# Performance work log

Hardware: AMD Instinct MI355X
Metric: run time of the kernel (lower is better)

## Reference

```python
import jax, jax.numpy as jnp
import numpy as np

D_MODEL = 1024
N_HEAD = 16
D_K = D_MODEL // N_HEAD
FFN = 4096
EPS = 1e-5


def setup_inputs() -> dict:
    key = jax.random.key(0)
    ks = jax.random.split(key, 12)
    s = 0.02
    return {
        "x": jax.random.normal(ks[0], (16, 512, D_MODEL), dtype=jnp.float32),
        "ln1_g": jnp.ones((D_MODEL,), jnp.float32),
        "ln1_b": jnp.zeros((D_MODEL,), jnp.float32),
        "w_q": jax.random.normal(ks[1], (D_MODEL, D_MODEL), jnp.float32) * s,
        "w_k": jax.random.normal(ks[2], (D_MODEL, D_MODEL), jnp.float32) * s,
        "w_v": jax.random.normal(ks[3], (D_MODEL, D_MODEL), jnp.float32) * s,
        "w_o": jax.random.normal(ks[4], (D_MODEL, D_MODEL), jnp.float32) * s,
        "b_o": jnp.zeros((D_MODEL,), jnp.float32),
        "ln2_g": jnp.ones((D_MODEL,), jnp.float32),
        "ln2_b": jnp.zeros((D_MODEL,), jnp.float32),
        "w1": jax.random.normal(ks[5], (D_MODEL, FFN), jnp.float32) * s,
        "b1": jnp.zeros((FFN,), jnp.float32),
        "w2": jax.random.normal(ks[6], (FFN, D_MODEL), jnp.float32) * s,
        "b2": jnp.zeros((D_MODEL,), jnp.float32),
    }


def layernorm(x, g, b):
    mu = jnp.mean(x, axis=-1, keepdims=True)
    var = jnp.mean((x - mu) ** 2, axis=-1, keepdims=True)
    return (x - mu) * jax.lax.rsqrt(var + EPS) * g + b


def reference(x, ln1_g, ln1_b, w_q, w_k, w_v, w_o, b_o, ln2_g, ln2_b, w1, b1, w2, b2):
    B, T, C = x.shape
    # --- attention sublayer (pre-LN) ---
    h = layernorm(x, ln1_g, ln1_b)
    # torch Linear: y = x @ W.T; here weights stored as (in, out) so y = x @ W
    q = (h @ w_q).reshape(B, T, N_HEAD, D_K).transpose(0, 2, 1, 3)  # bhtd
    k = (h @ w_k).reshape(B, T, N_HEAD, D_K).transpose(0, 2, 1, 3)
    v = (h @ w_v).reshape(B, T, N_HEAD, D_K).transpose(0, 2, 1, 3)
    scale = 1.0 / jnp.sqrt(jnp.float32(D_K))
    attn = jnp.einsum("bhqd,bhkd->bhqk", q, k) * scale  # [B,H,T,T]
    causal = jnp.tril(jnp.ones((T, T), bool))
    attn = jnp.where(causal[None, None], attn, -jnp.inf)
    attn = jax.nn.softmax(attn, axis=-1)
    out = jnp.einsum("bhqk,bhkd->bhqd", attn, v)
    out = out.transpose(0, 2, 1, 3).reshape(B, T, C)
    attn_out = out @ w_o + b_o
    x = x + attn_out
    # --- FFN sublayer (pre-LN) ---
    h = layernorm(x, ln2_g, ln2_b)
    ffn_out = jax.nn.gelu(h @ w1 + b1, approximate=False) @ w2 + b2
    return x + ffn_out
```

## Files before the change

### kernel.cpp

```cpp
#include <hip/hip_runtime.h>
#include <hip/hip_bf16.h>
#include <math.h>

#define D_MODEL 1024
#define FFN_DIM 4096
#define NHEAD 16
#define DK 64
#define BATCH 16
#define SEQ 512
#define ROWS (BATCH * SEQ)
#define QKV_N 3072

typedef short short8 __attribute__((ext_vector_type(8)));
typedef float f32x4 __attribute__((ext_vector_type(4)));

__device__ __forceinline__ float bf2f(short s) {
    return __uint_as_float(((unsigned)(unsigned short)s) << 16);
}
__device__ __forceinline__ short f2bf(float f) {
    unsigned u = __float_as_uint(f);
    u += 0x7fff + ((u >> 16) & 1);
    return (short)(u >> 16);
}

__device__ __forceinline__ int swz(int row, int col) {
    int s = (row ^ (row >> 3)) & 7;
    return row * 64 + ((((col >> 3) ^ s) << 3) | (col & 7));
}

__device__ __forceinline__ void gll16(const short* g, short* l) {
    __builtin_amdgcn_global_load_lds(
        (const __attribute__((address_space(1))) unsigned int*)g,
        (__attribute__((address_space(3))) unsigned int*)l, 16, 0, 0);
}

__global__ __launch_bounds__(256) void convT(const float* __restrict__ in,
                                             short* __restrict__ out,
                                             int K, int N) {
    __shared__ short t[64 * 64];
    const int tid = threadIdx.x;
    const int k0 = blockIdx.y * 64, n0 = blockIdx.x * 64;
    {
        const int r = tid >> 4;
        const int c4 = (tid & 15) * 4;
#pragma unroll
        for (int i = 0; i < 4; ++i) {
            const int row = i * 16 + r;
            float4 vv = *(const float4*)&in[(size_t)(k0 + row) * N + n0 + c4];
            t[swz(row, c4 + 0)] = f2bf(vv.x);
            t[swz(row, c4 + 1)] = f2bf(vv.y);
            t[swz(row, c4 + 2)] = f2bf(vv.z);
            t[swz(row, c4 + 3)] = f2bf(vv.w);
        }
    }
    __syncthreads();
    {
        const int n = tid >> 2;
        const int kc = (tid & 3) * 16;
        short tmp[16];
#pragma unroll
        for (int kk = 0; kk < 16; ++kk) tmp[kk] = t[swz(kc + kk, n)];
        short8 s0, s1;
#pragma unroll
        for (int j = 0; j < 8; ++j) { s0[j] = tmp[j]; s1[j] = tmp[8 + j]; }
        short* dst = &out[(size_t)(n0 + n) * K + k0 + kc];
        *(short8*)dst = s0;
        *(short8*)(dst + 8) = s1;
    }
}

__global__ __launch_bounds__(256) void ln_kernel(const float* __restrict__ x,
                                                 const float* __restrict__ g,
                                                 const float* __restrict__ beta,
                                                 short* __restrict__ out) {
    const int row = blockIdx.x;
    const int tid = threadIdx.x;
    const float4 xv = ((const float4*)(x + (size_t)row * D_MODEL))[tid];
    float s  = xv.x + xv.y + xv.z + xv.w;
    float s2 = xv.x * xv.x + xv.y * xv.y + xv.z * xv.z + xv.w * xv.w;
#pragma unroll
    for (int off = 32; off >= 1; off >>= 1) {
        s  += __shfl_down(s, off);
        s2 += __shfl_down(s2, off);
    }
    __shared__ float red[8];
    if ((tid & 63) == 0) { red[(tid >> 6) * 2] = s; red[(tid >> 6) * 2 + 1] = s2; }
    __syncthreads();
    s  = red[0] + red[2] + red[4] + red[6];
    s2 = red[1] + red[3] + red[5] + red[7];
    const float mu  = s * (1.0f / D_MODEL);
    const float var = s2 * (1.0f / D_MODEL) - mu * mu;
    const float r   = rsqrtf(var + 1e-5f);
    const int c = tid * 4;
    short4 ov;
    ov.x = f2bf((xv.x - mu) * r * g[c + 0] + beta[c + 0]);
    ov.y = f2bf((xv.y - mu) * r * g[c + 1] + beta[c + 1]);
    ov.z = f2bf((xv.z - mu) * r * g[c + 2] + beta[c + 2]);
    ov.w = f2bf((xv.w - mu) * r * g[c + 3] + beta[c + 3]);
    *(short4*)(out + (size_t)row * D_MODEL + c) = ov;
}

template <int MODE>
__global__ __launch_bounds__(256) void gemm128(
    const short* __restrict__ A, const short* __restrict__ Bt,
    int M, int N, int K, int ldc,
    const float* __restrict__ bias, const float* __restrict__ resid,
    float* __restrict__ outf, short* __restrict__ outb) {
    __shared__ __align__(16) short As[2][128 * 64];
    __shared__ __align__(16) short Bs[2][128 * 64];
    const int tid = threadIdx.x;
    const int w = tid >> 6, lane = tid & 63;
    const int lm = lane & 15, quad = lane >> 4;
    const int m0 = blockIdx.y * 128, n0 = blockIdx.x * 128;
    const int wm = (w & 1) * 64, wn = (w >> 1) * 64;

    const int srl = lane >> 3;
    const int gch = (lane & 7) ^ srl;
    const short* gA[4];
    const short* gB[4];
    int lofs[4];
#pragma unroll
    for (int j = 0; j < 4; ++j) {
        const int row = j * 32 + w * 8 + srl;
        gA[j] = A  + (size_t)(m0 + row) * K + gch * 8;
        gB[j] = Bt + (size_t)(n0 + row) * K + gch * 8;
        lofs[j] = (j * 32 + w * 8) * 64;
    }

    f32x4 acc[4][4];
#pragma unroll
    for (int i = 0; i < 4; ++i)
#pragma unroll
        for (int j = 0; j < 4; ++j) acc[i][j] = (f32x4){0.f, 0.f, 0.f, 0.f};

#pragma unroll
    for (int j = 0; j < 4; ++j) gll16(gA[j], &As[0][lofs[j]]);
#pragma unroll
    for (int j = 0; j < 4; ++j) gll16(gB[j], &Bs[0][lofs[j]]);

    int buf = 0;
    for (int k0 = 0; k0 < K; k0 += 64) {
        __syncthreads();
        if (k0 + 64 < K) {
#pragma unroll
            for (int j = 0; j < 4; ++j) gll16(gA[j] + k0 + 64, &As[buf ^ 1][lofs[j]]);
#pragma unroll
            for (int j = 0; j < 4; ++j) gll16(gB[j] + k0 + 64, &Bs[buf ^ 1][lofs[j]]);
        }
#pragma unroll
        for (int kk = 0; kk < 2; ++kk) {
            short8 af[4], bfr[4];
#pragma unroll
            for (int mm = 0; mm < 4; ++mm) {
                const int row = wm + mm * 16 + lm;
                const int ch = (kk * 4 + quad) ^ (row & 7);
                af[mm] = *(short8*)&As[buf][row * 64 + ch * 8];
            }
#pragma unroll
            for (int nn = 0; nn < 4; ++nn) {
                const int row = wn + nn * 16 + lm;
                const int ch = (kk * 4 + quad) ^ (row & 7);
                bfr[nn] = *(short8*)&Bs[buf][row * 64 + ch * 8];
            }
#pragma unroll
            for (int mm = 0; mm < 4; ++mm)
#pragma unroll
                for (int nn = 0; nn < 4; ++nn)
                    acc[mm][nn] = __builtin_amdgcn_mfma_f32_16x16x32_bf16(
                        af[mm], bfr[nn], acc[mm][nn], 0, 0, 0);
        }
        buf ^= 1;
    }

#pragma unroll
    for (int mm = 0; mm < 4; ++mm)
#pragma unroll
        for (int nn = 0; nn < 4; ++nn)
#pragma unroll
            for (int r = 0; r < 4; ++r) {
                const int row = m0 + wm + mm * 16 + quad * 4 + r;
                const int col = n0 + wn + nn * 16 + lm;
                const float vv = acc[mm][nn][r];
                if (MODE == 0) {
                    outb[(size_t)row * ldc + col] = f2bf(vv);
                } else if (MODE == 1) {
                    outf[(size_t)row * ldc + col] =
                        vv + bias[col] + resid[(size_t)row * ldc + col];
                } else {
                    const float gv = vv + bias[col];
                    const float u = 0.7978845608f * gv * (1.0f + 0.044715f * gv * gv);
                    const float ge = gv / (1.0f + __expf(-2.0f * u));
                    outb[(size_t)row * ldc + col] = f2bf(ge);
                }
            }
}

__global__ __launch_bounds__(256) void attn_mfma(const short* __restrict__ qkv,
                                                 short* __restrict__ o) {
    __shared__ __align__(16) short Ks[64 * 64];
    __shared__ __align__(16) short Vt[64 * 64];
    __shared__ __align__(16) short Ps[4][32 * 64];

    const int tid = threadIdx.x;
    const int qt = blockIdx.x, h = blockIdx.y, b = blockIdx.z;
    const int w = tid >> 6, lane = tid & 63;
    const int lm = lane & 15, quad = lane >> 4;

    const int sj  = tid >> 2;
    const int sd0 = (tid & 3) * 16;

    short8 aq[2][2];
#pragma unroll
    for (int m = 0; m < 2; ++m) {
        const short* qrow =
            qkv + (size_t)(b * SEQ + qt * 128 + w * 32 + m * 16 + lm) * QKV_N + h * DK;
#pragma unroll
        for (int kk = 0; kk < 2; ++kk) {
            short8 raw = *(const short8*)(qrow + kk * 32 + quad * 8);
            short8 sc;
#pragma unroll
            for (int j = 0; j < 8; ++j) sc[j] = f2bf(bf2f(raw[j]) * 0.125f);
            aq[m][kk] = sc;
        }
    }

    f32x4 accO[2][4];
#pragma unroll
    for (int m = 0; m < 2; ++m)
#pragma unroll
        for (int i = 0; i < 4; ++i) accO[m][i] = (f32x4){0.f, 0.f, 0.f, 0.f};
    float mrow[2][4], lrow[2][4];
#pragma unroll
    for (int m = 0; m < 2; ++m)
#pragma unroll
        for (int r = 0; r < 4; ++r) { mrow[m][r] = -1e30f; lrow[m][r] = 0.f; }

    short* pw = Ps[w];
    const int ktmax = 2 * qt + 1;

    for (int kt = 0; kt <= ktmax; ++kt) {
        __syncthreads();
        {
            const short* ksrc =
                qkv + (size_t)(b * SEQ + kt * 64 + sj) * QKV_N + D_MODEL + h * DK + sd0;
            short8 k0v = *(const short8*)ksrc;
            short8 k1v = *(const short8*)(ksrc + 8);
            *(short8*)&Ks[swz(sj, sd0)]     = k0v;
            *(short8*)&Ks[swz(sj, sd0 + 8)] = k1v;
            const short* vsrc =
                qkv + (size_t)(b * SEQ + kt * 64 + sj) * QKV_N + 2 * D_MODEL + h * DK + sd0;
            short8 v0v = *(const short8*)vsrc;
            short8 v1v = *(const short8*)(vsrc + 8);
#pragma unroll
            for (int dd = 0; dd < 8; ++dd) Vt[swz(sd0 + dd, sj)]     = v0v[dd];
#pragma unroll
            for (int dd = 0; dd < 8; ++dd) Vt[swz(sd0 + 8 + dd, sj)] = v1v[dd];
        }
        __syncthreads();

        bool live[2];
#pragma unroll
        for (int m = 0; m < 2; ++m) {
            const int rowmin = qt * 128 + w * 32 + m * 16;
            live[m] = (kt * 64 <= rowmin + 15);
            if (!live[m]) continue;
            const bool needmask = (kt * 64 + 63 > rowmin);

            f32x4 sacc[4];
#pragma unroll
            for (int nn = 0; nn < 4; ++nn) sacc[nn] = (f32x4){0.f, 0.f, 0.f, 0.f};
#pragma unroll
            for (int kk = 0; kk < 2; ++kk)
#pragma unroll
                for (int nn = 0; nn < 4; ++nn) {
                    short8 bfrag = *(short8*)&Ks[swz(nn * 16 + lm, kk * 32 + quad * 8)];
                    sacc[nn] = __builtin_amdgcn_mfma_f32_16x16x32_bf16(
                        aq[m][kk], bfrag, sacc[nn], 0, 0, 0);
                }

            if (needmask) {
#pragma unroll
                for (int nn = 0; nn < 4; ++nn) {
                    const int kg = kt * 64 + nn * 16 + lm;
#pragma unroll
                    for (int r = 0; r < 4; ++r) {
                        const int qg = rowmin + quad * 4 + r;
                        if (kg > qg) sacc[nn][r] = -1e30f;
                    }
                }
            }

            float mnew[4], alpha[4], rsum[4];
#pragma unroll
            for (int r = 0; r < 4; ++r) {
                float mx = fmaxf(fmaxf(sacc[0][r], sacc[1][r]),
                                 fmaxf(sacc[2][r], sacc[3][r]));
#pragma unroll
                for (int msk = 1; msk <= 8; msk <<= 1) mx = fmaxf(mx, __shfl_xor(mx, msk));
                mnew[r] = fmaxf(mrow[m][r], mx);
                alpha[r] = __expf(mrow[m][r] - mnew[r]);
                rsum[r] = 0.f;
            }
#pragma unroll
            for (int nn = 0; nn < 4; ++nn)
#pragma unroll
                for (int r = 0; r < 4; ++r) {
                    const float p = __expf(sacc[nn][r] - mnew[r]);
                    sacc[nn][r] = p;
                    rsum[r] += p;
                }
#pragma unroll
            for (int r = 0; r < 4; ++r) {
#pragma unroll
                for (int msk = 1; msk <= 8; msk <<= 1) rsum[r] += __shfl_xor(rsum[r], msk);
                lrow[m][r] = lrow[m][r] * alpha[r] + rsum[r];
                mrow[m][r] = mnew[r];
            }
#pragma unroll
            for (int nn = 0; nn < 4; ++nn)
#pragma unroll
                for (int r = 0; r < 4; ++r) accO[m][nn][r] *= alpha[r];

#pragma unroll
            for (int nn = 0; nn < 4; ++nn)
#pragma unroll
                for (int r = 0; r < 4; ++r)
                    pw[swz(m * 16 + quad * 4 + r, nn * 16 + lm)] = f2bf(sacc[nn][r]);
        }

#pragma unroll
        for (int kk = 0; kk < 2; ++kk) {
            short8 bfr[4];
#pragma unroll
            for (int nn = 0; nn < 4; ++nn)
                bfr[nn] = *(short8*)&Vt[swz(nn * 16 + lm, kk * 32 + quad * 8)];
#pragma unroll
            for (int m = 0; m < 2; ++m) {
                if (!live[m]) continue;
                short8 afrag = *(short8*)&pw[swz(m * 16 + lm, kk * 32 + quad * 8)];
#pragma unroll
                for (int nn = 0; nn < 4; ++nn)
                    accO[m][nn] = __builtin_amdgcn_mfma_f32_16x16x32_bf16(
                        afrag, bfr[nn], accO[m][nn], 0, 0, 0);
            }
        }
    }

#pragma unroll
    for (int m = 0; m < 2; ++m)
#pragma unroll
        for (int r = 0; r < 4; ++r) {
            const float invl = 1.0f / lrow[m][r];
            const int row = b * SEQ + qt * 128 + w * 32 + m * 16 + quad * 4 + r;
#pragma unroll
            for (int nn = 0; nn < 4; ++nn)
                o[(size_t)row * D_MODEL + h * DK + nn * 16 + lm] =
                    f2bf(accO[m][nn][r] * invl);
        }
}

extern "C" void kernel_launch(void* const* d_in, const int* in_sizes, int n_in,
                              void* d_out, int out_size, void* d_ws, size_t ws_size,
                              hipStream_t stream) {
    const float* x     = (const float*)d_in[0];
    const float* ln1_g = (const float*)d_in[1];
    const float* ln1_b = (const float*)d_in[2];
    const float* w_q   = (const float*)d_in[3];
    const float* w_k   = (const float*)d_in[4];
    const float* w_v   = (const float*)d_in[5];
    const float* w_o   = (const float*)d_in[6];
    const float* b_o   = (const float*)d_in[7];
    const float* ln2_g = (const float*)d_in[8];
    const float* ln2_b = (const float*)d_in[9];
    const float* w1    = (const float*)d_in[10];
    const float* b1    = (const float*)d_in[11];
    const float* w2    = (const float*)d_in[12];
    const float* b2    = (const float*)d_in[13];
    float* out = (float*)d_out;

    char* ws = (char*)d_ws;
    size_t off = 0;
    auto alloc = [&](size_t bytes) {
        char* p = ws + off;
        off += (bytes + 255) & ~(size_t)255;
        return p;
    };
    short* h_bf   = (short*)alloc((size_t)ROWS * D_MODEL * 2);
    short* qkv_bf = (short*)alloc((size_t)ROWS * QKV_N * 2);
    short* a_bf   = (short*)alloc((size_t)ROWS * D_MODEL * 2);
    float* x1     = (float*)alloc((size_t)ROWS * D_MODEL * 4);
    short* wqkvT  = (short*)alloc((size_t)QKV_N * D_MODEL * 2);
    short* woT    = (short*)alloc((size_t)D_MODEL * D_MODEL * 2);
    short* w1T    = (short*)alloc((size_t)D_MODEL * FFN_DIM * 2);
    short* w2T    = (short*)alloc((size_t)FFN_DIM * D_MODEL * 2);
    short* g1_bf  = qkv_bf;

    convT<<<dim3(16, 16), 256, 0, stream>>>(w_q, wqkvT, D_MODEL, D_MODEL);
    convT<<<dim3(16, 16), 256, 0, stream>>>(w_k, wqkvT + (size_t)D_MODEL * D_MODEL,
                                            D_MODEL, D_MODEL);
    convT<<<dim3(16, 16), 256, 0, stream>>>(w_v, wqkvT + (size_t)2 * D_MODEL * D_MODEL,
                                            D_MODEL, D_MODEL);
    convT<<<dim3(16, 16), 256, 0, stream>>>(w_o, woT, D_MODEL, D_MODEL);
    convT<<<dim3(64, 16), 256, 0, stream>>>(w1, w1T, D_MODEL, FFN_DIM);
    convT<<<dim3(16, 64), 256, 0, stream>>>(w2, w2T, FFN_DIM, D_MODEL);

    ln_kernel<<<ROWS, 256, 0, stream>>>(x, ln1_g, ln1_b, h_bf);

    gemm128<0><<<dim3(QKV_N / 128, ROWS / 128), 256, 0, stream>>>(
        h_bf, wqkvT, ROWS, QKV_N, D_MODEL, QKV_N,
        nullptr, nullptr, nullptr, qkv_bf);

    attn_mfma<<<dim3(SEQ / 128, NHEAD, BATCH), 256, 0, stream>>>(qkv_bf, a_bf);

    gemm128<1><<<dim3(D_MODEL / 128, ROWS / 128), 256, 0, stream>>>(
        a_bf, woT, ROWS, D_MODEL, D_MODEL, D_MODEL, b_o, x, x1, nullptr);

    ln_kernel<<<ROWS, 256, 0, stream>>>(x1, ln2_g, ln2_b, h_bf);

    gemm128<2><<<dim3(FFN_DIM / 128, ROWS / 128), 256, 0, stream>>>(
        h_bf, w1T, ROWS, FFN_DIM, D_MODEL, FFN_DIM, b1, nullptr, nullptr, g1_bf);

    gemm128<1><<<dim3(D_MODEL / 128, ROWS / 128), 256, 0, stream>>>(
        g1_bf, w2T, ROWS, D_MODEL, FFN_DIM, D_MODEL, b2, x1, out, nullptr);
}
```

Before: 511.6 us.

## Pre-shuffle weights into MFMA fragment order and load B directly from global

Weight conversion now writes bf16 weights in a packed per-16-column, per-32-k fragment layout that matches the MFMA B-operand register layout. The GEMM drops the B shared-memory tiles and their async copies and has each lane read its B fragments straight from global memory, one 16-byte load per fragment. This halves LDS usage and removes B staging, which could raise occupancy. The cost is that B reads are no longer shared through LDS between the two waves that use the same columns, and the global loads are issued synchronously inside the inner loop, so their latency is not prefetched a stage ahead.

Result: no change. 504.5 us (-1.4%).

```diff
diff --git a/kernel.cpp b/kernel.cpp
--- a/kernel.cpp
+++ b/kernel.cpp
@@ -34,39 +34,20 @@
         (__attribute__((address_space(3))) unsigned int*)l, 16, 0, 0);
 }
 
-__global__ __launch_bounds__(256) void convT(const float* __restrict__ in,
-                                             short* __restrict__ out,
-                                             int K, int N) {
-    __shared__ short t[64 * 64];
+__global__ __launch_bounds__(256) void convShuf(const float* __restrict__ in,
+                                                short* __restrict__ out,
+                                                int K, int N) {
     const int tid = threadIdx.x;
-    const int k0 = blockIdx.y * 64, n0 = blockIdx.x * 64;
-    {
-        const int r = tid >> 4;
-        const int c4 = (tid & 15) * 4;
-#pragma unroll
-        for (int i = 0; i < 4; ++i) {
-            const int row = i * 16 + r;
-            float4 vv = *(const float4*)&in[(size_t)(k0 + row) * N + n0 + c4];
-            t[swz(row, c4 + 0)] = f2bf(vv.x);
-            t[swz(row, c4 + 1)] = f2bf(vv.y);
-            t[swz(row, c4 + 2)] = f2bf(vv.z);
-            t[swz(row, c4 + 3)] = f2bf(vv.w);
-        }
-    }
-    __syncthreads();
-    {
-        const int n = tid >> 2;
-        const int kc = (tid & 3) * 16;
-        short tmp[16];
-#pragma unroll
-        for (int kk = 0; kk < 16; ++kk) tmp[kk] = t[swz(kc + kk, n)];
-        short8 s0, s1;
-#pragma unroll
-        for (int j = 0; j < 8; ++j) { s0[j] = tmp[j]; s1[j] = tmp[8 + j]; }
-        short* dst = &out[(size_t)(n0 + n) * K + k0 + kc];
-        *(short8*)dst = s0;
-        *(short8*)(dst + 8) = s1;
-    }
+    const int lane = tid & 63, fl = tid >> 6;
+    const int lm = lane & 15, quad = lane >> 4;
+    const int nt = blockIdx.x;
+    const int kc = blockIdx.y * 4 + fl;
+    const int n = nt * 16 + lm;
+    const int kb = kc * 32 + quad * 8;
+    short8 v;
+#pragma unroll
+    for (int j = 0; j < 8; ++j) v[j] = f2bf(in[(size_t)(kb + j) * N + n]);
+    *(short8*)&out[((size_t)nt * (K / 32) + kc) * 512 + lane * 8] = v;
 }
 
 __global__ __launch_bounds__(256) void ln_kernel(const float* __restrict__ x,
@@ -102,31 +83,34 @@
 
 template <int MODE>
 __global__ __launch_bounds__(256) void gemm128(
-    const short* __restrict__ A, const short* __restrict__ Bt,
+    const short* __restrict__ A, const short* __restrict__ Bp,
     int M, int N, int K, int ldc,
     const float* __restrict__ bias, const float* __restrict__ resid,
     float* __restrict__ outf, short* __restrict__ outb) {
     __shared__ __align__(16) short As[2][128 * 64];
-    __shared__ __align__(16) short Bs[2][128 * 64];
     const int tid = threadIdx.x;
     const int w = tid >> 6, lane = tid & 63;
     const int lm = lane & 15, quad = lane >> 4;
     const int m0 = blockIdx.y * 128, n0 = blockIdx.x * 128;
     const int wm = (w & 1) * 64, wn = (w >> 1) * 64;
+    const int KC = K / 32;
 
     const int srl = lane >> 3;
     const int gch = (lane & 7) ^ srl;
     const short* gA[4];
-    const short* gB[4];
     int lofs[4];
 #pragma unroll
     for (int j = 0; j < 4; ++j) {
         const int row = j * 32 + w * 8 + srl;
-        gA[j] = A  + (size_t)(m0 + row) * K + gch * 8;
-        gB[j] = Bt + (size_t)(n0 + row) * K + gch * 8;
+        gA[j] = A + (size_t)(m0 + row) * K + gch * 8;
         lofs[j] = (j * 32 + w * 8) * 64;
     }
 
+    const short* bptr[4];
+#pragma unroll
+    for (int nn = 0; nn < 4; ++nn)
+        bptr[nn] = Bp + ((size_t)((n0 + wn) / 16 + nn) * KC) * 512 + lane * 8;
+
     f32x4 acc[4][4];
 #pragma unroll
     for (int i = 0; i < 4; ++i)
@@ -135,8 +119,6 @@
 
 #pragma unroll
     for (int j = 0; j < 4; ++j) gll16(gA[j], &As[0][lofs[j]]);
-#pragma unroll
-    for (int j = 0; j < 4; ++j) gll16(gB[j], &Bs[0][lofs[j]]);
 
     int buf = 0;
     for (int k0 = 0; k0 < K; k0 += 64) {
@@ -144,23 +126,19 @@
         if (k0 + 64 < K) {
 #pragma unroll
             for (int j = 0; j < 4; ++j) gll16(gA[j] + k0 + 64, &As[buf ^ 1][lofs[j]]);
-#pragma unroll
-            for (int j = 0; j < 4; ++j) gll16(gB[j] + k0 + 64, &Bs[buf ^ 1][lofs[j]]);
         }
 #pragma unroll
         for (int kk = 0; kk < 2; ++kk) {
+            const int kc = (k0 >> 5) + kk;
             short8 af[4], bfr[4];
+#pragma unroll
+            for (int nn = 0; nn < 4; ++nn)
+                bfr[nn] = *(const short8*)(bptr[nn] + (size_t)kc * 512);
 #pragma unroll
             for (int mm = 0; mm < 4; ++mm) {
                 const int row = wm + mm * 16 + lm;
                 const int ch = (kk * 4 + quad) ^ (row & 7);
                 af[mm] = *(short8*)&As[buf][row * 64 + ch * 8];
-            }
-#pragma unroll
-            for (int nn = 0; nn < 4; ++nn) {
-                const int row = wn + nn * 16 + lm;
-                const int ch = (kk * 4 + quad) ^ (row & 7);
-                bfr[nn] = *(short8*)&Bs[buf][row * 64 + ch * 8];
             }
 #pragma unroll
             for (int mm = 0; mm < 4; ++mm)
@@ -389,37 +367,42 @@
     short* qkv_bf = (short*)alloc((size_t)ROWS * QKV_N * 2);
     short* a_bf   = (short*)alloc((size_t)ROWS * D_MODEL * 2);
     float* x1     = (float*)alloc((size_t)ROWS * D_MODEL * 4);
-    short* wqkvT  = (short*)alloc((size_t)QKV_N * D_MODEL * 2);
-    short* woT    = (short*)alloc((size_t)D_MODEL * D_MODEL * 2);
-    short* w1T    = (short*)alloc((size_t)D_MODEL * FFN_DIM * 2);
-    short* w2T    = (short*)alloc((size_t)FFN_DIM * D_MODEL * 2);
+    short* wqkvP  = (short*)alloc((size_t)QKV_N * D_MODEL * 2);
+    short* woP    = (short*)alloc((size_t)D_MODEL * D_MODEL * 2);
+    short* w1P    = (short*)alloc((size_t)D_MODEL * FFN_DIM * 2);
+    short* w2P    = (short*)alloc((size_t)FFN_DIM * D_MODEL * 2);
     short* g1_bf  = qkv_bf;
 
-    convT<<<dim3(16, 16), 256, 0, stream>>>(w_q, wqkvT, D_MODEL, D_MODEL);
-    convT<<<dim3(16, 16), 256, 0, stream>>>(w_k, wqkvT + (size_t)D_MODEL * D_MODEL,
-                                            D_MODEL, D_MODEL);
-    convT<<<dim3(16, 16), 256, 0, stream>>>(w_v, wqkvT + (size_t)2 * D_MODEL * D_MODEL,
-                                            D_MODEL, D_MODEL);
-    convT<<<dim3(16, 16), 256, 0, stream>>>(w_o, woT, D_MODEL, D_MODEL);
-    convT<<<dim3(64, 16), 256, 0, stream>>>(w1, w1T, D_MODEL, FFN_DIM);
-    convT<<<dim3(16, 64), 256, 0, stream>>>(w2, w2T, FFN_DIM, D_MODEL);
+    const int KC1 = D_MODEL / 32;
+    convShuf<<<dim3(D_MODEL / 16, D_MODEL / 128), 256, 0, stream>>>(
+        w_q, wqkvP, D_MODEL, D_MODEL);
+    convShuf<<<dim3(D_MODEL / 16, D_MODEL / 128), 256, 0, stream>>>(
+        w_k, wqkvP + (size_t)64 * KC1 * 512, D_MODEL, D_MODEL);
+    convShuf<<<dim3(D_MODEL / 16, D_MODEL / 128), 256, 0, stream>>>(
+        w_v, wqkvP + (size_t)128 * KC1 * 512, D_MODEL, D_MODEL);
+    convShuf<<<dim3(D_MODEL / 16, D_MODEL / 128), 256, 0, stream>>>(
+        w_o, woP, D_MODEL, D_MODEL);
+    convShuf<<<dim3(FFN_DIM / 16, D_MODEL / 128), 256, 0, stream>>>(
+        w1, w1P, D_MODEL, FFN_DIM);
+    convShuf<<<dim3(D_MODEL / 16, FFN_DIM / 128), 256, 0, stream>>>(
+        w2, w2P, FFN_DIM, D_MODEL);
 
     ln_kernel<<<ROWS, 256, 0, stream>>>(x, ln1_g, ln1_b, h_bf);
 
     gemm128<0><<<dim3(QKV_N / 128, ROWS / 128), 256, 0, stream>>>(
-        h_bf, wqkvT, ROWS, QKV_N, D_MODEL, QKV_N,
+        h_bf, wqkvP, ROWS, QKV_N, D_MODEL, QKV_N,
         nullptr, nullptr, nullptr, qkv_bf);
 
     attn_mfma<<<dim3(SEQ / 128, NHEAD, BATCH), 256, 0, stream>>>(qkv_bf, a_bf);
 
     gemm128<1><<<dim3(D_MODEL / 128, ROWS / 128), 256, 0, stream>>>(
-        a_bf, woT, ROWS, D_MODEL, D_MODEL, D_MODEL, b_o, x, x1, nullptr);
+        a_bf, woP, ROWS, D_MODEL, D_MODEL, D_MODEL, b_o, x, x1, nullptr);
 
     ln_kernel<<<ROWS, 256, 0, stream>>>(x1, ln2_g, ln2_b, h_bf);
 
     gemm128<2><<<dim3(FFN_DIM / 128, ROWS / 128), 256, 0, stream>>>(
-        h_bf, w1T, ROWS, FFN_DIM, D_MODEL, FFN_DIM, b1, nullptr, nullptr, g1_bf);
+        h_bf, w1P, ROWS, FFN_DIM, D_MODEL, FFN_DIM, b1, nullptr, nullptr, g1_bf);
 
     gemm128<1><<<dim3(D_MODEL / 128, ROWS / 128), 256, 0, stream>>>(
-        g1_bf, w2T, ROWS, D_MODEL, FFN_DIM, D_MODEL, b2, x1, out, nullptr);
-}
+        g1_bf, w2P, ROWS, D_MODEL, FFN_DIM, D_MODEL, b2, x1, out, nullptr);
+}
```
